# Performance work log

Measured on AMD Instinct MI355X. Metric: run time of the kernel, lower is better.

The kernel has to match this reference:

```python
import jax, jax.numpy as jnp
import numpy as np

EPS = 1e-06

def setup_inputs() -> dict:
    key = jax.random.key(0)
    k1, k2, k3, k4, k5 = jax.random.split(key, 5)
    B, T, D, Dv = 4, 2048, 128, 128
    q = jax.random.normal(k1, (B, T, D), dtype=jnp.float32)
    k = jax.random.normal(k2, (B, T, D), dtype=jnp.float32)
    v = jax.random.normal(k3, (B, T, Dv), dtype=jnp.float32)
    # phi = nn.Linear(dim, dim) followed by ELU; torch Linear default init ~ U(-1/sqrt(D), 1/sqrt(D))
    lim = 1.0 / np.sqrt(D)
    W_phi = jax.random.uniform(k4, (D, D), minval=-lim, maxval=lim, dtype=jnp.float32)
    b_phi = jax.random.uniform(k5, (D,), minval=-lim, maxval=lim, dtype=jnp.float32)
    return {"q": q, "k": k, "v": v, "W_phi": W_phi, "b_phi": b_phi}

def reference(q, k, v, W_phi, b_phi):
    # feature map: phi(x) = ELU(x @ W^T + b) + 1  (positive features)
    def phi(x):
        return jax.nn.elu(jnp.einsum('btd,ed->bte', x, W_phi) + b_phi) + 1.0

    Q = phi(q)                      # [B,T,D]
    K = phi(k)                      # [B,T,D]
    # causal recurrent state (zero initial state since h=None):
    # z_t = sum_{tau<=t} K_tau                 -> [B,T,D]
    # s_t = sum_{tau<=t} K_tau (outer) v_tau   -> [B,T,D,Dv]
    z = jnp.cumsum(K, axis=1)
    s = jnp.cumsum(K[..., :, None] * v[..., None, :], axis=1)
    den = jnp.einsum('btd,btd->bt', Q, z) + EPS          # [B,T]
    out = jnp.einsum('btd,btde->bte', Q, s) / den[..., None]  # [B,T,Dv]
    return out
```

## Files before the change

### kernel.cpp

```cpp
#include <hip/hip_runtime.h>
#include <hip/hip_bf16.h>

#define BB 4
#define TT 2048
#define DD 128
#define CHK 64
#define NCHK 32
#define NCHKS (BB*NCHK)

typedef __attribute__((ext_vector_type(8))) short  bf16x8;
typedef __attribute__((ext_vector_type(4))) float  f32x4;

#define MFMA(a,b,c) __builtin_amdgcn_mfma_f32_16x16x32_bf16(a, b, c, 0, 0, 0)

__device__ __forceinline__ short f2b(float f) {
    union { float f; unsigned u; } x; x.f = f;
    unsigned r = x.u + 0x7fffu + ((x.u >> 16) & 1u);
    return (short)(r >> 16);
}
__device__ __forceinline__ float b2f(short s) {
    union { unsigned u; float f; } x; x.u = ((unsigned)(unsigned short)s) << 16;
    return x.f;
}
__device__ __forceinline__ bf16x8 cvt8(const float* p) {
    float4 a = *(const float4*)p, b = *(const float4*)(p + 4);
    bf16x8 r;
    r[0]=f2b(a.x); r[1]=f2b(a.y); r[2]=f2b(a.z); r[3]=f2b(a.w);
    r[4]=f2b(b.x); r[5]=f2b(b.y); r[6]=f2b(b.z); r[7]=f2b(b.w);
    return r;
}

__global__ __launch_bounds__(256) void k1_chunk(const float* __restrict__ q,
                                                const float* __restrict__ kin,
                                                const float* __restrict__ vin,
                                                const float* __restrict__ W,
                                                const float* __restrict__ bias,
                                                short* __restrict__ Ss_g,
                                                float* __restrict__ zc_g,
                                                short* __restrict__ vT_g,
                                                short* __restrict__ Qf_g,
                                                short* __restrict__ Kf_g) {
    int c = blockIdx.x >> 1, h = blockIdx.x & 1;
    const float* qc = q   + (size_t)c * CHK * DD;
    const float* kc = kin + (size_t)c * CHK * DD;
    const float* vc = vin + (size_t)c * CHK * DD;

    __shared__ __align__(16) short Wl  [DD][DD + 8];
    __shared__ __align__(16) short KfT [DD][CHK + 8];
    __shared__ __align__(16) short vT  [CHK][CHK + 8];
    __shared__ __align__(16) short stage[CHK][DD + 8];

    int tid = threadIdx.x, lane = tid & 63, w = tid >> 6;
    int l15 = lane & 15, l4 = lane >> 4;
    const f32x4 z4 = {0.f, 0.f, 0.f, 0.f};

    bf16x8 afk[4], afq[4];
    {
        int row = 16 * w + l15;
        #pragma unroll
        for (int kk = 0; kk < 4; ++kk) afk[kk] = cvt8(kc + row * DD + kk * 32 + l4 * 8);
        if (h) {
            #pragma unroll
            for (int kk = 0; kk < 4; ++kk) afq[kk] = cvt8(qc + row * DD + kk * 32 + l4 * 8);
        }
    }
    #pragma unroll
    for (int it = 0; it < 16; ++it) {
        int i = tid + it * 256;
        int row = i >> 5, c4 = (i & 31) * 4;
        float4 v = *(const float4*)(W + (size_t)row * DD + c4);
        unsigned lo = (unsigned short)f2b(v.x) | ((unsigned)(unsigned short)f2b(v.y) << 16);
        unsigned hi = (unsigned short)f2b(v.z) | ((unsigned)(unsigned short)f2b(v.w) << 16);
        uint2 p; p.x = lo; p.y = hi;
        *(uint2*)&Wl[row][c4] = p;
    }
    #pragma unroll
    for (int it = 0; it < 4; ++it) {
        int i = tid + it * 256;
        int t = i >> 4, c4 = (i & 15) * 4;
        float4 vv = *(const float4*)(vc + t * DD + 64 * h + c4);
        vT[c4 + 0][t] = f2b(vv.x); vT[c4 + 1][t] = f2b(vv.y);
        vT[c4 + 2][t] = f2b(vv.z); vT[c4 + 3][t] = f2b(vv.w);
    }
    __syncthreads();

    #pragma unroll
    for (int n = 0; n < 8; ++n) {
        int e = 16 * n + l15;
        f32x4 d = z4;
        #pragma unroll
        for (int kk = 0; kk < 4; ++kk) {
            bf16x8 bw = *(const bf16x8*)&Wl[e][kk * 32 + l4 * 8];
            d = MFMA(afk[kk], bw, d);
        }
        float bv = bias[e];
        #pragma unroll
        for (int j = 0; j < 4; ++j) {
            float zv = d[j] + bv;
            short r = f2b((zv > 0.f) ? (zv + 1.f) : __expf(zv));
            int t = 16 * w + l4 * 4 + j;
            KfT[e][t] = r;
            if (h == 0) stage[t][e] = r;
        }
    }
    if (h) {
        #pragma unroll
        for (int n = 0; n < 8; ++n) {
            int e = 16 * n + l15;
            f32x4 d = z4;
            #pragma unroll
            for (int kk = 0; kk < 4; ++kk) {
                bf16x8 bw = *(const bf16x8*)&Wl[e][kk * 32 + l4 * 8];
                d = MFMA(afq[kk], bw, d);
            }
            float bv = bias[e];
            #pragma unroll
            for (int j = 0; j < 4; ++j) {
                float zv = d[j] + bv;
                stage[16 * w + l4 * 4 + j][e] = f2b((zv > 0.f) ? (zv + 1.f) : __expf(zv));
            }
        }
    }
    __syncthreads();

    {
        short* dst = (h ? Qf_g : Kf_g) + (size_t)c * CHK * DD;
        #pragma unroll
        for (int it = 0; it < 4; ++it) {
            int i = tid + it * 256;
            int t = i >> 4, u = (i & 15) * 8;
            *(bf16x8*)(dst + t * DD + u) = *(const bf16x8*)&stage[t][u];
        }
    }
    if (h == 0 && tid < DD) {
        float s = 0.f;
        #pragma unroll
        for (int t8 = 0; t8 < CHK / 8; ++t8) {
            bf16x8 kv = *(const bf16x8*)&KfT[tid][t8 * 8];
            #pragma unroll
            for (int j = 0; j < 8; ++j) s += b2f(kv[j]);
        }
        zc_g[(size_t)c * DD + tid] = s;
    }
    #pragma unroll
    for (int it = 0; it < 2; ++it) {
        int i = tid + it * 256;
        int e = i >> 3, t0 = (i & 7) * 8;
        *(bf16x8*)(vT_g + (size_t)c * DD * CHK + (64 * h + e) * CHK + t0) =
            *(const bf16x8*)&vT[e][t0];
    }

    f32x4 sacc[2][4];
    #pragma unroll
    for (int mi = 0; mi < 2; ++mi)
        #pragma unroll
        for (int n = 0; n < 4; ++n) sacc[mi][n] = z4;
    #pragma unroll
    for (int kk = 0; kk < 2; ++kk) {
        bf16x8 afr[2];
        #pragma unroll
        for (int mi = 0; mi < 2; ++mi)
            afr[mi] = *(const bf16x8*)&KfT[16 * (2 * w + mi) + l15][kk * 32 + l4 * 8];
        #pragma unroll
        for (int n = 0; n < 4; ++n) {
            bf16x8 bfr = *(const bf16x8*)&vT[16 * n + l15][kk * 32 + l4 * 8];
            sacc[0][n] = MFMA(afr[0], bfr, sacc[0][n]);
            sacc[1][n] = MFMA(afr[1], bfr, sacc[1][n]);
        }
    }
    __syncthreads();

    #pragma unroll
    for (int mi = 0; mi < 2; ++mi)
        #pragma unroll
        for (int n = 0; n < 4; ++n) {
            int e = 16 * n + l15;
            #pragma unroll
            for (int j = 0; j < 4; ++j)
                stage[e][16 * (2 * w + mi) + l4 * 4 + j] = f2b(sacc[mi][n][j]);
        }
    __syncthreads();

    short* dst = Ss_g + (size_t)c * DD * DD + (size_t)(64 * h) * DD;
    #pragma unroll
    for (int it = 0; it < 4; ++it) {
        int i = tid + it * 256;
        int e = i >> 4, u = (i & 15) * 8;
        *(bf16x8*)(dst + e * DD + u) = *(const bf16x8*)&stage[e][u];
    }
}

__global__ __launch_bounds__(128) void k2_scan(const short* __restrict__ Ss_g,
                                               const float* __restrict__ zc_g,
                                               short* __restrict__ Sp_g,
                                               float* __restrict__ zp_g) {
    int e = blockIdx.x & 127, b = blockIdx.x >> 7;
    int d = threadIdx.x;
    size_t base = ((size_t)(b * NCHK) * DD + e) * DD + d;
    const size_t stride = (size_t)DD * DD;

    float vals[NCHK];
    #pragma unroll
    for (int c2 = 0; c2 < NCHK; ++c2) vals[c2] = b2f(Ss_g[base + c2 * stride]);
    float run = 0.f;
    #pragma unroll
    for (int c2 = 0; c2 < NCHK; ++c2) {
        Sp_g[base + c2 * stride] = f2b(run);
        run += vals[c2];
    }
    if (e == 0) {
        float vz[NCHK];
        #pragma unroll
        for (int c2 = 0; c2 < NCHK; ++c2) vz[c2] = zc_g[(size_t)(b * NCHK + c2) * DD + d];
        float rz = 0.f;
        #pragma unroll
        for (int c2 = 0; c2 < NCHK; ++c2) {
            zp_g[(size_t)(b * NCHK + c2) * DD + d] = rz;
            rz += vz[c2];
        }
    }
}

__global__ __launch_bounds__(256) void k3_out(const short* __restrict__ Qf_g,
                                              const short* __restrict__ Kf_g,
                                              const short* __restrict__ Sp_g,
                                              const float* __restrict__ zp_g,
                                              const short* __restrict__ vT_g,
                                              float* __restrict__ out) {
    int c = blockIdx.x >> 1, h = blockIdx.x & 1;

    __shared__ __align__(16) short Qf[CHK][DD + 8];
    __shared__ __align__(16) short Kf[CHK][DD + 8];
    __shared__ __align__(16) short Ps[CHK][CHK + 8];
    __shared__ float zs[DD];
    __shared__ float den[CHK];

    int tid = threadIdx.x, lane = tid & 63, w = tid >> 6;
    int l15 = lane & 15, l4 = lane >> 4;
    const f32x4 z4 = {0.f, 0.f, 0.f, 0.f};

    if (tid < DD) zs[tid] = zp_g[(size_t)c * DD + tid];

    {
        const short* srcq = Qf_g + (size_t)c * CHK * DD;
        const short* srck = Kf_g + (size_t)c * CHK * DD;
        #pragma unroll
        for (int it = 0; it < 4; ++it) {
            int i = tid + it * 256;
            int t = i >> 4, u = (i & 15) * 8;
            *(bf16x8*)&Qf[t][u] = *(const bf16x8*)(srcq + t * DD + u);
            *(bf16x8*)&Kf[t][u] = *(const bf16x8*)(srck + t * DD + u);
        }
    }
    __syncthreads();

    bf16x8 aq[4];
    #pragma unroll
    for (int kk = 0; kk < 4; ++kk)
        aq[kk] = *(const bf16x8*)&Qf[16 * w + l15][kk * 32 + l4 * 8];
    #pragma unroll
    for (int n2 = 0; n2 < 4; ++n2) {
        f32x4 p = z4;
        #pragma unroll
        for (int kk = 0; kk < 4; ++kk) {
            bf16x8 bk = *(const bf16x8*)&Kf[16 * n2 + l15][kk * 32 + l4 * 8];
            p = MFMA(aq[kk], bk, p);
        }
        int t2 = 16 * n2 + l15;
        #pragma unroll
        for (int j = 0; j < 4; ++j) {
            int t = 16 * w + l4 * 4 + j;
            Ps[t][t2] = (t2 <= t) ? f2b(p[j]) : (short)0;
        }
    }
    __syncthreads();

    if (tid < CHK) {
        float s = 1e-6f;
        #pragma unroll
        for (int t8 = 0; t8 < CHK / 8; ++t8) {
            bf16x8 pv = *(const bf16x8*)&Ps[tid][t8 * 8];
            #pragma unroll
            for (int j = 0; j < 8; ++j) s += b2f(pv[j]);
        }
        #pragma unroll
        for (int d8 = 0; d8 < DD / 8; ++d8) {
            bf16x8 qv = *(const bf16x8*)&Qf[tid][d8 * 8];
            #pragma unroll
            for (int j = 0; j < 8; ++j) s += b2f(qv[j]) * zs[d8 * 8 + j];
        }
        den[tid] = s;
    }

    bf16x8 ap[2];
    #pragma unroll
    for (int kk = 0; kk < 2; ++kk)
        ap[kk] = *(const bf16x8*)&Ps[16 * w + l15][kk * 32 + l4 * 8];

    const short* Sp  = Sp_g + (size_t)c * DD * DD;
    const short* vTg = vT_g + (size_t)c * DD * CHK;
    f32x4 oacc[4];
    #pragma unroll
    for (int n = 0; n < 4; ++n) oacc[n] = z4;
    #pragma unroll
    for (int n = 0; n < 4; ++n) {
        int e = 64 * h + 16 * n + l15;
        #pragma unroll
        for (int kk = 0; kk < 4; ++kk) {
            bf16x8 bs = *(const bf16x8*)(Sp + e * DD + kk * 32 + l4 * 8);
            oacc[n] = MFMA(aq[kk], bs, oacc[n]);
        }
        #pragma unroll
        for (int kk = 0; kk < 2; ++kk) {
            bf16x8 bv = *(const bf16x8*)(vTg + e * CHK + kk * 32 + l4 * 8);
            oacc[n] = MFMA(ap[kk], bv, oacc[n]);
        }
    }
    __syncthreads();

    float* oc = out + (size_t)c * CHK * DD;
    float invs[4];
    #pragma unroll
    for (int j = 0; j < 4; ++j) invs[j] = 1.0f / den[16 * w + l4 * 4 + j];
    #pragma unroll
    for (int n = 0; n < 4; ++n) {
        int e = 64 * h + 16 * n + l15;
        #pragma unroll
        for (int j = 0; j < 4; ++j) {
            int t = 16 * w + l4 * 4 + j;
            oc[t * DD + e] = oacc[n][j] * invs[j];
        }
    }
}

extern "C" void kernel_launch(void* const* d_in, const int* in_sizes, int n_in,
                              void* d_out, int out_size, void* d_ws, size_t ws_size,
                              hipStream_t stream) {
    const float* q  = (const float*)d_in[0];
    const float* k  = (const float*)d_in[1];
    const float* v  = (const float*)d_in[2];
    const float* W  = (const float*)d_in[3];
    const float* bi = (const float*)d_in[4];
    float* out = (float*)d_out;

    float* zc_g = (float*)d_ws;
    float* zp_g = zc_g + (size_t)NCHKS * DD;
    short* Ss_g = (short*)(zp_g + (size_t)NCHKS * DD);
    short* Sp_g = Ss_g + (size_t)NCHKS * DD * DD;
    short* vT_g = Sp_g + (size_t)NCHKS * DD * DD;
    short* Qf_g = vT_g + (size_t)NCHKS * DD * CHK;
    short* Kf_g = Qf_g + (size_t)NCHKS * CHK * DD;

    k1_chunk<<<2 * NCHKS, 256, 0, stream>>>(q, k, v, W, bi, Ss_g, zc_g, vT_g, Qf_g, Kf_g);
    k2_scan<<<512, 128, 0, stream>>>(Ss_g, zc_g, Sp_g, zp_g);
    k3_out<<<2 * NCHKS, 256, 0, stream>>>(Qf_g, Kf_g, Sp_g, zp_g, vT_g, out);
}
```

Before: 27.31 us.

## Fuse chunk-state prefix scan into output kernel, drop separate scan launch

Removes the standalone scan kernel. Each output block now sums the preceding chunk states (and z vectors) for its own half of the state directly from the per-chunk buffers into shared memory. Blocks are launched in reverse chunk order so the most expensive late chunks start first. This saves a kernel launch and the write/read round trip of the prefix buffer. In exchange the redundant summation work is quadratic in chunk count, with up to 31 serial 16 KB loads per block.

Result: slower. 40.60 us (+48.7%).

```diff
diff --git a/kernel.cpp b/kernel.cpp
--- a/kernel.cpp
+++ b/kernel.cpp
@@ -190,47 +190,20 @@
     }
 }
 
-__global__ __launch_bounds__(128) void k2_scan(const short* __restrict__ Ss_g,
-                                               const float* __restrict__ zc_g,
-                                               short* __restrict__ Sp_g,
-                                               float* __restrict__ zp_g) {
-    int e = blockIdx.x & 127, b = blockIdx.x >> 7;
-    int d = threadIdx.x;
-    size_t base = ((size_t)(b * NCHK) * DD + e) * DD + d;
-    const size_t stride = (size_t)DD * DD;
-
-    float vals[NCHK];
-    #pragma unroll
-    for (int c2 = 0; c2 < NCHK; ++c2) vals[c2] = b2f(Ss_g[base + c2 * stride]);
-    float run = 0.f;
-    #pragma unroll
-    for (int c2 = 0; c2 < NCHK; ++c2) {
-        Sp_g[base + c2 * stride] = f2b(run);
-        run += vals[c2];
-    }
-    if (e == 0) {
-        float vz[NCHK];
-        #pragma unroll
-        for (int c2 = 0; c2 < NCHK; ++c2) vz[c2] = zc_g[(size_t)(b * NCHK + c2) * DD + d];
-        float rz = 0.f;
-        #pragma unroll
-        for (int c2 = 0; c2 < NCHK; ++c2) {
-            zp_g[(size_t)(b * NCHK + c2) * DD + d] = rz;
-            rz += vz[c2];
-        }
-    }
-}
-
 __global__ __launch_bounds__(256) void k3_out(const short* __restrict__ Qf_g,
                                               const short* __restrict__ Kf_g,
-                                              const short* __restrict__ Sp_g,
-                                              const float* __restrict__ zp_g,
+                                              const short* __restrict__ Ss_g,
+                                              const float* __restrict__ zc_g,
                                               const short* __restrict__ vT_g,
                                               float* __restrict__ out) {
-    int c = blockIdx.x >> 1, h = blockIdx.x & 1;
+    int c = (NCHKS - 1) - (blockIdx.x >> 1);
+    int h = blockIdx.x & 1;
+    int cb = c & (NCHK - 1);
+    int b0 = c & ~(NCHK - 1);
 
     __shared__ __align__(16) short Qf[CHK][DD + 8];
     __shared__ __align__(16) short Kf[CHK][DD + 8];
+    __shared__ __align__(16) short Sp[CHK][DD + 8];
     __shared__ __align__(16) short Ps[CHK][CHK + 8];
     __shared__ float zs[DD];
     __shared__ float den[CHK];
@@ -238,8 +211,6 @@
     int tid = threadIdx.x, lane = tid & 63, w = tid >> 6;
     int l15 = lane & 15, l4 = lane >> 4;
     const f32x4 z4 = {0.f, 0.f, 0.f, 0.f};
-
-    if (tid < DD) zs[tid] = zp_g[(size_t)c * DD + tid];
 
     {
         const short* srcq = Qf_g + (size_t)c * CHK * DD;
@@ -252,6 +223,40 @@
             *(bf16x8*)&Kf[t][u] = *(const bf16x8*)(srck + t * DD + u);
         }
     }
+
+    if (tid < DD) {
+        float s = 0.f;
+        for (int c2 = 0; c2 < cb; ++c2)
+            s += zc_g[(size_t)(b0 + c2) * DD + tid];
+        zs[tid] = s;
+    }
+
+    {
+        float acc0[8] = {0,0,0,0,0,0,0,0}, acc1[8] = {0,0,0,0,0,0,0,0};
+        float acc2[8] = {0,0,0,0,0,0,0,0}, acc3[8] = {0,0,0,0,0,0,0,0};
+        int e0 = tid >> 4, u0 = (tid & 15) * 8;
+        int e1 = (tid + 256) >> 4, u1 = u0;
+        int e2 = (tid + 512) >> 4, u2 = u0;
+        int e3 = (tid + 768) >> 4, u3 = u0;
+        const short* base = Ss_g + (size_t)64 * h * DD;
+        for (int c2 = 0; c2 < cb; ++c2) {
+            const short* src = base + (size_t)(b0 + c2) * DD * DD;
+            bf16x8 v0 = *(const bf16x8*)(src + e0 * DD + u0);
+            bf16x8 v1 = *(const bf16x8*)(src + e1 * DD + u1);
+            bf16x8 v2 = *(const bf16x8*)(src + e2 * DD + u2);
+            bf16x8 v3 = *(const bf16x8*)(src + e3 * DD + u3);
+            #pragma unroll
+            for (int j = 0; j < 8; ++j) {
+                acc0[j] += b2f(v0[j]); acc1[j] += b2f(v1[j]);
+                acc2[j] += b2f(v2[j]); acc3[j] += b2f(v3[j]);
+            }
+        }
+        #pragma unroll
+        for (int j = 0; j < 8; ++j) {
+            Sp[e0][u0 + j] = f2b(acc0[j]); Sp[e1][u1 + j] = f2b(acc1[j]);
+            Sp[e2][u2 + j] = f2b(acc2[j]); Sp[e3][u3 + j] = f2b(acc3[j]);
+        }
+    }
     __syncthreads();
 
     bf16x8 aq[4];
@@ -297,17 +302,17 @@
     for (int kk = 0; kk < 2; ++kk)
         ap[kk] = *(const bf16x8*)&Ps[16 * w + l15][kk * 32 + l4 * 8];
 
-    const short* Sp  = Sp_g + (size_t)c * DD * DD;
     const short* vTg = vT_g + (size_t)c * DD * CHK;
     f32x4 oacc[4];
     #pragma unroll
     for (int n = 0; n < 4; ++n) oacc[n] = z4;
     #pragma unroll
     for (int n = 0; n < 4; ++n) {
-        int e = 64 * h + 16 * n + l15;
+        int el = 16 * n + l15;
+        int e  = 64 * h + el;
         #pragma unroll
         for (int kk = 0; kk < 4; ++kk) {
-            bf16x8 bs = *(const bf16x8*)(Sp + e * DD + kk * 32 + l4 * 8);
+            bf16x8 bs = *(const bf16x8*)&Sp[el][kk * 32 + l4 * 8];
             oacc[n] = MFMA(aq[kk], bs, oacc[n]);
         }
         #pragma unroll
@@ -344,14 +349,11 @@
     float* out = (float*)d_out;
 
     float* zc_g = (float*)d_ws;
-    float* zp_g = zc_g + (size_t)NCHKS * DD;
-    short* Ss_g = (short*)(zp_g + (size_t)NCHKS * DD);
-    short* Sp_g = Ss_g + (size_t)NCHKS * DD * DD;
-    short* vT_g = Sp_g + (size_t)NCHKS * DD * DD;
+    short* Ss_g = (short*)(zc_g + (size_t)NCHKS * DD);
+    short* vT_g = Ss_g + (size_t)NCHKS * DD * DD;
     short* Qf_g = vT_g + (size_t)NCHKS * DD * CHK;
     short* Kf_g = Qf_g + (size_t)NCHKS * CHK * DD;
 
     k1_chunk<<<2 * NCHKS, 256, 0, stream>>>(q, k, v, W, bi, Ss_g, zc_g, vT_g, Qf_g, Kf_g);
-    k2_scan<<<512, 128, 0, stream>>>(Ss_g, zc_g, Sp_g, zp_g);
-    k3_out<<<2 * NCHKS, 256, 0, stream>>>(Qf_g, Kf_g, Sp_g, zp_g, vT_g, out);
-}
+    k3_out<<<2 * NCHKS, 256, 0, stream>>>(Qf_g, Kf_g, Ss_g, zc_g, vT_g, out);
+}
```
